# Performance work log

Hardware: AMD Instinct MI355X
Metric: run time of the kernel (lower is better)

## Reference

```python
import jax, jax.numpy as jnp
import numpy as np


def _time_encoding(t, hidden_dim):
    # Sinusoidal continuous-time encoding: t [B,T] -> [B,T,H]
    half = hidden_dim // 2
    freqs = jnp.exp(-jnp.arange(half, dtype=t.dtype) * (np.log(10000.0) / half))
    ang = t[..., None] * freqs  # [B,T,half]
    return jnp.concatenate([jnp.sin(ang), jnp.cos(ang)], axis=-1)


def _gru(x_tbh, w_ih, w_hh, b_ih, b_hh):
    # PyTorch-convention GRU over time-major input [T,B,H]
    B = x_tbh.shape[1]
    H = w_hh.shape[1]
    h0 = jnp.zeros((B, H), x_tbh.dtype)

    def step(h, x):
        gi = x @ w_ih.T + b_ih
        gh = h @ w_hh.T + b_hh
        i_r, i_z, i_n = jnp.split(gi, 3, axis=-1)
        h_r, h_z, h_n = jnp.split(gh, 3, axis=-1)
        r = jax.nn.sigmoid(i_r + h_r)
        z = jax.nn.sigmoid(i_z + h_z)
        n = jnp.tanh(i_n + r * h_n)
        h_new = (1.0 - z) * n + z * h
        return h_new, h_new

    _, ys = jax.lax.scan(step, h0, x_tbh)
    return ys  # [T,B,H]


def setup_inputs():
    key = jax.random.key(0)
    ks = jax.random.split(key, 8)
    B, T, D, H = 32, 256, 64, 128
    x = jax.random.normal(ks[0], (B, T, D), jnp.float32)
    missing_mask = (jax.random.uniform(ks[1], (B, T, D)) < 0.5).astype(jnp.float32)
    visit_time = jnp.cumsum(jax.random.uniform(ks[2], (B, T), jnp.float32) * 2.0, axis=1)
    time_delta = jnp.zeros((B, T), jnp.float32)
    lengths = jax.random.randint(ks[3], (B,), T // 2, T + 1).astype(jnp.int32)
    lengths = lengths.at[0].set(T)  # pad_packed returns max(lengths) steps; pin to T
    sensor_embed = jax.random.normal(ks[4], (D, H), jnp.float32) * 0.02
    k = 1.0 / np.sqrt(H)
    gru_w_ih = jax.random.uniform(ks[5], (3 * H, H), jnp.float32, -k, k)
    gru_w_hh = jax.random.uniform(ks[6], (3 * H, H), jnp.float32, -k, k)
    gru_b_ih = jax.random.uniform(ks[7], (3 * H,), jnp.float32, -k, k)
    gru_b_hh = jnp.zeros((3 * H,), jnp.float32)
    return dict(x=x, missing_mask=missing_mask, visit_time=visit_time,
                time_delta=time_delta, lengths=lengths, sensor_embed=sensor_embed,
                gru_w_ih=gru_w_ih, gru_w_hh=gru_w_hh, gru_b_ih=gru_b_ih, gru_b_hh=gru_b_hh)


def reference(x, missing_mask, visit_time, time_delta, lengths, sensor_embed,
              gru_w_ih, gru_w_hh, gru_b_ih, gru_b_hh):
    B, T, D = x.shape
    H = sensor_embed.shape[1]
    observed = 1.0 - missing_mask                                   # [B,T,D]
    # sensor tokens: per-(t,sensor) embedding scaled by value, zeroed if missing
    sensor_tokens = x[..., None] * sensor_embed[None, None] * observed[..., None]  # [B,T,D,H]
    presence = observed.mean(axis=1)                                # [B,D]
    sim = jax.nn.relu(sensor_embed @ sensor_embed.T)                # [D,D]
    adj = presence[:, :, None] * presence[:, None, :] * sim[None]   # [B,D,D]
    adj = adj + jnp.eye(D, dtype=x.dtype)[None]
    adj = adj / jnp.maximum(adj.sum(axis=-1, keepdims=True), 1e-6)
    graph_tokens = jnp.einsum('bij,btjh->btih', adj, sensor_tokens) # [B,T,D,H]
    visit_repr = graph_tokens.mean(axis=2) + _time_encoding(visit_time, H)  # [B,T,H]
    # dropout is identity in eval mode
    ys = _gru(jnp.swapaxes(visit_repr, 0, 1), gru_w_ih, gru_w_hh, gru_b_ih, gru_b_hh)
    out = jnp.swapaxes(ys, 0, 1)                                    # [B,T,H]
    # pad_packed_sequence semantics: zeros beyond each sequence length
    mask = (jnp.arange(T)[None, :] < lengths[:, None])[..., None]
    return out * mask
```

## Files before the change

### kernel.cpp

```cpp
#include <hip/hip_runtime.h>
#include <hip/hip_bf16.h>

#define B_ 32
#define T_ 256
#define D_ 64
#define H_ 128
#define G_ 384

typedef _Float16 half8 __attribute__((ext_vector_type(8)));
typedef _Float16 half4v __attribute__((ext_vector_type(4)));
typedef float float4v __attribute__((ext_vector_type(4)));

__device__ __forceinline__ float fsigmoid(float x){ return 1.0f/(1.0f+__expf(-x)); }
__device__ __forceinline__ float ftanh_(float x){ return 1.0f - 2.0f/(1.0f+__expf(2.0f*x)); }

#define BAR() do{ asm volatile("s_waitcnt lgkmcnt(0)" ::: "memory"); \
                  __builtin_amdgcn_s_barrier(); \
                  asm volatile("" ::: "memory"); } while(0)

__global__ void __launch_bounds__(256) adj_k(const float* mm, const float* E,
                                             float* wcol){
  int b = blockIdx.x;
  int tid = threadIdx.x;
  int d = tid & 63, q = tid >> 6;
  __shared__ float spp[4][64];
  __shared__ float sp[64];
  __shared__ float sE[64*129];
  __shared__ float ssim[64*65];
  __shared__ float srs[64];
  float p = 0.0f;
  for (int t = q*64; t < q*64+64; t++) p += 1.0f - mm[(b*T_ + t)*D_ + d];
  spp[q][d] = p;
  for (int i = tid; i < D_*H_; i += 256){ int r = i >> 7, c = i & 127; sE[r*129+c] = E[i]; }
  __syncthreads();
  if (tid < 64) sp[tid] = (spp[0][tid]+spp[1][tid]+spp[2][tid]+spp[3][tid]) * (1.0f/T_);
  __syncthreads();
  float rowE[128];
  #pragma unroll
  for (int k = 0; k < 128; k++) rowE[k] = sE[d*129+k];
  for (int i = q*16; i < q*16+16; i++){
    float s = 0.0f;
    #pragma unroll
    for (int k = 0; k < 128; k++) s += rowE[k]*sE[i*129+k];
    ssim[d*65+i] = fmaxf(s, 0.0f);
  }
  __syncthreads();
  if (tid < 64){
    float rs = 0.0f;
    for (int j = 0; j < 64; j++) rs += sp[j]*ssim[tid*65+j];
    srs[tid] = fmaxf(sp[tid]*rs + 1.0f, 1e-6f);
  }
  __syncthreads();
  if (tid < 64){
    float s = 0.0f;
    for (int i = 0; i < 64; i++) s += sp[i]*ssim[tid*65+i]/srs[i];
    wcol[b*64 + tid] = sp[tid]*s + 1.0f/srs[tid];
  }
}

#define AVP 72
#define VRP 136
#define SEP 132
__global__ void __launch_bounds__(512,1) gi_k(const float* x, const float* mm,
                                              const float* vt, const float* E,
                                              const float* wih, const float* bih,
                                              const float* bhh, const float* wcol,
                                              _Float16* gi3){
  int bid = blockIdx.x;
  int b = bid >> 3, t0 = (bid & 7)*32;
  int tid = threadIdx.x;
  int w = tid >> 6, l = tid & 63;
  int lq = l >> 4, lm = l & 15;

  __shared__ __align__(16) _Float16 av[32*AVP];
  __shared__ __align__(16) _Float16 vrA[32*VRP];
  __shared__ __align__(16) _Float16 sEl[64*SEP];
  __shared__ float sVt[32];

  {
    int i = tid*4, t = i >> 6, d4 = i & 63;
    long src = (long)(b*T_ + t0 + t)*D_ + d4;
    float4 xv = *(const float4*)&x[src];
    float4 mv = *(const float4*)&mm[src];
    float4 wv = *(const float4*)&wcol[b*D_ + d4];
    half4v h;
    h[0]=(_Float16)(xv.x*(1.0f-mv.x)*wv.x*(1.0f/64));
    h[1]=(_Float16)(xv.y*(1.0f-mv.y)*wv.y*(1.0f/64));
    h[2]=(_Float16)(xv.z*(1.0f-mv.z)*wv.z*(1.0f/64));
    h[3]=(_Float16)(xv.w*(1.0f-mv.w)*wv.w*(1.0f/64));
    *(half4v*)&av[t*AVP + d4] = h;
  }
  {
    int r = tid >> 3, c0 = (tid & 7)*16;
    #pragma unroll
    for (int g = 0; g < 4; g++){
      float4 v = *(const float4*)&E[r*H_ + c0 + g*4];
      half4v h;
      h[0]=(_Float16)v.x; h[1]=(_Float16)v.y; h[2]=(_Float16)v.z; h[3]=(_Float16)v.w;
      *(half4v*)&sEl[r*SEP + c0 + g*4] = h;
    }
  }
  if (tid < 32) sVt[tid] = vt[b*T_ + t0 + tid];
  __syncthreads();

  half8 bE[2];
  #pragma unroll
  for (int kc = 0; kc < 2; kc++){
    half8 f;
    #pragma unroll
    for (int jj = 0; jj < 8; jj++)
      f[jj] = sEl[(kc*32 + lq*8 + jj)*SEP + 16*w + lm];
    bE[kc] = f;
  }

  float4v accA[2] = {{0,0,0,0},{0,0,0,0}};
  #pragma unroll
  for (int kc = 0; kc < 2; kc++){
    #pragma unroll
    for (int mt = 0; mt < 2; mt++){
      half8 a = *(const half8*)&av[(mt*16+lm)*AVP + kc*32 + lq*8];
      accA[mt] = __builtin_amdgcn_mfma_f32_16x16x32_f16(a, bE[kc], accA[mt], 0,0,0);
    }
  }
  {
    int h = 16*w + lm;
    float fr = __expf(-(float)(h & 63) * 0.14391157f);
    #pragma unroll
    for (int mt = 0; mt < 2; mt++){
      #pragma unroll
      for (int r = 0; r < 4; r++){
        int tl = mt*16 + lq*4 + r;
        float ang = sVt[tl] * fr;
        float e = (h < 64) ? __sinf(ang) : __cosf(ang);
        vrA[tl*VRP + h] = (_Float16)(accA[mt][r] + e);
      }
    }
  }
  __syncthreads();

  half8 bW[3][4]; float biW[3];
  #pragma unroll
  for (int q = 0; q < 3; q++){
    int g = 16*(3*w + q) + lm;
    biW[q] = bih[g] + (g < 2*H_ ? bhh[g] : 0.0f);
    #pragma unroll
    for (int kc = 0; kc < 4; kc++){
      const float* src = &wih[(long)g*H_ + kc*32 + lq*8];
      float4 x0 = *(const float4*)src;
      float4 x1 = *(const float4*)(src+4);
      half8 f;
      f[0]=(_Float16)x0.x; f[1]=(_Float16)x0.y; f[2]=(_Float16)x0.z; f[3]=(_Float16)x0.w;
      f[4]=(_Float16)x1.x; f[5]=(_Float16)x1.y; f[6]=(_Float16)x1.z; f[7]=(_Float16)x1.w;
      bW[q][kc] = f;
    }
  }
  float4v cB[2][3];
  #pragma unroll
  for (int mt = 0; mt < 2; mt++)
    #pragma unroll
    for (int q = 0; q < 3; q++) cB[mt][q] = (float4v){0,0,0,0};
  #pragma unroll
  for (int kc = 0; kc < 4; kc++){
    #pragma unroll
    for (int mt = 0; mt < 2; mt++){
      half8 a = *(const half8*)&vrA[(mt*16+lm)*VRP + kc*32 + lq*8];
      #pragma unroll
      for (int q = 0; q < 3; q++)
        cB[mt][q] = __builtin_amdgcn_mfma_f32_16x16x32_f16(a, bW[q][kc], cB[mt][q], 0,0,0);
    }
  }
  #pragma unroll
  for (int mt = 0; mt < 2; mt++){
    #pragma unroll
    for (int q = 0; q < 3; q++){
      int g = 16*(3*w + q) + lm;
      int tb = t0 + mt*16 + lq*4;
      half4v hv;
      hv[0]=(_Float16)(cB[mt][q][0] + biW[q]); hv[1]=(_Float16)(cB[mt][q][1] + biW[q]);
      hv[2]=(_Float16)(cB[mt][q][2] + biW[q]); hv[3]=(_Float16)(cB[mt][q][3] + biW[q]);
      *(half4v*)&gi3[((long)(b*G_ + g))*T_ + tb] = hv;
    }
  }
}

__global__ void __launch_bounds__(256,1) gru_k(const _Float16* gi3, const float* whh,
                                               const float* bhh, const int* lengths,
                                               float* out){
  int b = blockIdx.x;
  int tid = threadIdx.x;
  int w = tid >> 6, l = tid & 63;
  int lq = l >> 4, lm = l & 15;
  int len = lengths[b];
  bool gate = (l < 32);
  int j = 32*w + l;

  __shared__ __align__(16) _Float16 hb[2][H_];

  half8 bfrag[6][4];
  #pragma unroll
  for (int i = 0; i < 6; i++){
    int row = 32*w + (i>>1)*H_ + (i&1)*16 + lm;
    #pragma unroll
    for (int kc = 0; kc < 4; kc++){
      const float* src = &whh[(long)row*H_ + kc*32 + lq*8];
      float4 x0 = *(const float4*)src;
      float4 x1 = *(const float4*)(src+4);
      half8 f;
      f[0]=(_Float16)x0.x; f[1]=(_Float16)x0.y; f[2]=(_Float16)x0.z; f[3]=(_Float16)x0.w;
      f[4]=(_Float16)x1.x; f[5]=(_Float16)x1.y; f[6]=(_Float16)x1.z; f[7]=(_Float16)x1.w;
      bfrag[i][kc] = f;
    }
  }
  float bn_ = 0.0f;
  const _Float16* pr = nullptr; const _Float16* pz; const _Float16* pn;
  if (gate){
    bn_ = bhh[2*H_ + j];
    pr = gi3 + ((long)b*G_ + j)*T_;
    pz = pr + (long)H_*T_;
    pn = pr + (long)2*H_*T_;
  }
  if (tid < H_){ hb[0][tid] = (_Float16)0.0f; hb[1][tid] = (_Float16)0.0f; }

  float gr[2][8], gz[2][8], gn[2][8];
  if (gate){
    half8 a = *(const half8*)(pr);
    half8 bv = *(const half8*)(pz);
    half8 cv = *(const half8*)(pn);
    #pragma unroll
    for (int i = 0; i < 8; i++){ gr[0][i]=(float)a[i]; gz[0][i]=(float)bv[i]; gn[0][i]=(float)cv[i]; }
  }
  __syncthreads();

  float hval = 0.0f;
  float ho[8];
  int cb = 0;
  for (int c = 0; c < 32; c++){
    if (gate && c+1 < 32){
      int nb2 = (c+1)*8;
      half8 a = *(const half8*)(pr+nb2);
      half8 bv = *(const half8*)(pz+nb2);
      half8 cv = *(const half8*)(pn+nb2);
      int nc = cb^1;
      #pragma unroll
      for (int i = 0; i < 8; i++){ gr[nc][i]=(float)a[i]; gz[nc][i]=(float)bv[i]; gn[nc][i]=(float)cv[i]; }
    }
    #pragma unroll
    for (int i = 0; i < 8; i++){
      int rp = i & 1;
      half8 a0v = *(const half8*)&hb[rp][0*32 + lq*8];
      half8 a1v = *(const half8*)&hb[rp][1*32 + lq*8];
      half8 a2v = *(const half8*)&hb[rp][2*32 + lq*8];
      half8 a3v = *(const half8*)&hb[rp][3*32 + lq*8];
      float4v cc[6];
      #pragma unroll
      for (int q = 0; q < 6; q++) cc[q] = (float4v){0,0,0,0};
      #pragma unroll
      for (int q = 0; q < 6; q++) cc[q] = __builtin_amdgcn_mfma_f32_16x16x32_f16(a0v, bfrag[q][0], cc[q], 0,0,0);
      #pragma unroll
      for (int q = 0; q < 6; q++) cc[q] = __builtin_amdgcn_mfma_f32_16x16x32_f16(a1v, bfrag[q][1], cc[q], 0,0,0);
      #pragma unroll
      for (int q = 0; q < 6; q++) cc[q] = __builtin_amdgcn_mfma_f32_16x16x32_f16(a2v, bfrag[q][2], cc[q], 0,0,0);
      #pragma unroll
      for (int q = 0; q < 6; q++) cc[q] = __builtin_amdgcn_mfma_f32_16x16x32_f16(a3v, bfrag[q][3], cc[q], 0,0,0);
      float ghr = (l & 16) ? cc[1][0] : cc[0][0];
      float ghz = (l & 16) ? cc[3][0] : cc[2][0];
      float ghn = (l & 16) ? cc[5][0] : cc[4][0];
      if (gate){
        float r = fsigmoid(gr[cb][i] + ghr);
        float z = fsigmoid(gz[cb][i] + ghz);
        float n = ftanh_(gn[cb][i] + r*(ghn + bn_));
        hval = (1.0f - z)*n + z*hval;
        hb[rp^1][j] = (_Float16)hval;
        ho[i] = (c*8 + i < len) ? hval : 0.0f;
      }
      BAR();
    }
    if (gate){
      long ob = ((long)b*T_ + c*8)*H_ + j;
      #pragma unroll
      for (int i = 0; i < 8; i++) out[ob + (long)i*H_] = ho[i];
    }
    cb ^= 1;
  }
}

extern "C" void kernel_launch(void* const* d_in, const int* in_sizes, int n_in,
                              void* d_out, int out_size, void* d_ws, size_t ws_size,
                              hipStream_t stream) {
  char* base = (char*)d_ws;
  size_t off = 0;
  auto alloc = [&](size_t bytes)->void*{
    void* p = base + off; off = (off + bytes + 255) & ~(size_t)255; return p;
  };
  float*     wcol = (float*)alloc((size_t)B_*D_*4);
  _Float16*  gi3  = (_Float16*)alloc((size_t)B_*G_*T_*2);
  if (off > ws_size) return;

  const float* x   = (const float*)d_in[0];
  const float* mm  = (const float*)d_in[1];
  const float* vt  = (const float*)d_in[2];
  const int*   len = (const int*)d_in[4];
  const float* E   = (const float*)d_in[5];
  const float* wih = (const float*)d_in[6];
  const float* whh = (const float*)d_in[7];
  const float* bih = (const float*)d_in[8];
  const float* bhh = (const float*)d_in[9];

  adj_k<<<dim3(B_),dim3(256),0,stream>>>(mm, E, wcol);
  gi_k<<<dim3(256),dim3(512),0,stream>>>(x, mm, vt, E, wih, bih, bhh, wcol, gi3);
  gru_k<<<dim3(B_),dim3(256),0,stream>>>(gi3, whh, bhh, len, (float*)d_out);
}
```

Baseline: 256.6 us.

## Split GRU recurrent matmul K dimension across two wave groups

Doubles the GRU block to 512 threads and splits the hidden-state reduction across two groups of four waves. Each group computes half of the recurrent matmul, writes partial sums to shared memory, and the first group combines them before the gate math. This aims to shorten the per-step MFMA dependency chain in the latency-bound recurrence. In exchange it adds an extra barrier and LDS round trip per timestep.

```diff
diff --git a/kernel.cpp b/kernel.cpp
--- a/kernel.cpp
+++ b/kernel.cpp
@@ -10,6 +10,7 @@
 typedef _Float16 half8 __attribute__((ext_vector_type(8)));
 typedef _Float16 half4v __attribute__((ext_vector_type(4)));
 typedef float float4v __attribute__((ext_vector_type(4)));
+typedef float float2v __attribute__((ext_vector_type(2)));
 
 __device__ __forceinline__ float fsigmoid(float x){ return 1.0f/(1.0f+__expf(-x)); }
 __device__ __forceinline__ float ftanh_(float x){ return 1.0f - 2.0f/(1.0f+__expf(2.0f*x)); }
@@ -183,32 +184,37 @@
   }
 }
 
-__global__ void __launch_bounds__(256,1) gru_k(const _Float16* gi3, const float* whh,
+__global__ void __launch_bounds__(512,1) gru_k(const _Float16* gi3, const float* whh,
                                                const float* bhh, const int* lengths,
                                                float* out){
   int b = blockIdx.x;
   int tid = threadIdx.x;
   int w = tid >> 6, l = tid & 63;
+  int ww = w & 3, kh = w >> 2;
   int lq = l >> 4, lm = l & 15;
   int len = lengths[b];
-  bool gate = (l < 32);
-  int j = 32*w + l;
+  bool part = (l < 32);
+  bool gate = part && (kh == 0);
+  int j = 32*ww + l;
 
   __shared__ __align__(16) _Float16 hb[2][H_];
-
-  half8 bfrag[6][4];
+  __shared__ __align__(16) float2v ghrz[2][H_];
+  __shared__ float ghn_[2][H_];
+
+  half8 bfrag[6][2];
   #pragma unroll
   for (int i = 0; i < 6; i++){
-    int row = 32*w + (i>>1)*H_ + (i&1)*16 + lm;
-    #pragma unroll
-    for (int kc = 0; kc < 4; kc++){
+    int row = 32*ww + (i>>1)*H_ + (i&1)*16 + lm;
+    #pragma unroll
+    for (int k2 = 0; k2 < 2; k2++){
+      int kc = 2*kh + k2;
       const float* src = &whh[(long)row*H_ + kc*32 + lq*8];
       float4 x0 = *(const float4*)src;
       float4 x1 = *(const float4*)(src+4);
       half8 f;
       f[0]=(_Float16)x0.x; f[1]=(_Float16)x0.y; f[2]=(_Float16)x0.z; f[3]=(_Float16)x0.w;
       f[4]=(_Float16)x1.x; f[5]=(_Float16)x1.y; f[6]=(_Float16)x1.z; f[7]=(_Float16)x1.w;
-      bfrag[i][kc] = f;
+      bfrag[i][k2] = f;
     }
   }
   float bn_ = 0.0f;
@@ -247,10 +253,8 @@
     #pragma unroll
     for (int i = 0; i < 8; i++){
       int rp = i & 1;
-      half8 a0v = *(const half8*)&hb[rp][0*32 + lq*8];
-      half8 a1v = *(const half8*)&hb[rp][1*32 + lq*8];
-      half8 a2v = *(const half8*)&hb[rp][2*32 + lq*8];
-      half8 a3v = *(const half8*)&hb[rp][3*32 + lq*8];
+      half8 a0v = *(const half8*)&hb[rp][kh*64 + 0*32 + lq*8];
+      half8 a1v = *(const half8*)&hb[rp][kh*64 + 1*32 + lq*8];
       float4v cc[6];
       #pragma unroll
       for (int q = 0; q < 6; q++) cc[q] = (float4v){0,0,0,0};
@@ -258,17 +262,20 @@
       for (int q = 0; q < 6; q++) cc[q] = __builtin_amdgcn_mfma_f32_16x16x32_f16(a0v, bfrag[q][0], cc[q], 0,0,0);
       #pragma unroll
       for (int q = 0; q < 6; q++) cc[q] = __builtin_amdgcn_mfma_f32_16x16x32_f16(a1v, bfrag[q][1], cc[q], 0,0,0);
-      #pragma unroll
-      for (int q = 0; q < 6; q++) cc[q] = __builtin_amdgcn_mfma_f32_16x16x32_f16(a2v, bfrag[q][2], cc[q], 0,0,0);
-      #pragma unroll
-      for (int q = 0; q < 6; q++) cc[q] = __builtin_amdgcn_mfma_f32_16x16x32_f16(a3v, bfrag[q][3], cc[q], 0,0,0);
-      float ghr = (l & 16) ? cc[1][0] : cc[0][0];
-      float ghz = (l & 16) ? cc[3][0] : cc[2][0];
-      float ghn = (l & 16) ? cc[5][0] : cc[4][0];
+      if (part){
+        float pr_ = (l & 16) ? cc[1][0] : cc[0][0];
+        float pz_ = (l & 16) ? cc[3][0] : cc[2][0];
+        float pn_ = (l & 16) ? cc[5][0] : cc[4][0];
+        ghrz[kh][j] = (float2v){pr_, pz_};
+        ghn_[kh][j] = pn_;
+      }
+      BAR();
       if (gate){
-        float r = fsigmoid(gr[cb][i] + ghr);
-        float z = fsigmoid(gz[cb][i] + ghz);
-        float n = ftanh_(gn[cb][i] + r*(ghn + bn_));
+        float2v rz0 = ghrz[0][j], rz1 = ghrz[1][j];
+        float n0 = ghn_[0][j],  n1 = ghn_[1][j];
+        float r = fsigmoid(gr[cb][i] + rz0[0] + rz1[0]);
+        float z = fsigmoid(gz[cb][i] + rz0[1] + rz1[1]);
+        float n = ftanh_(gn[cb][i] + r*(n0 + n1 + bn_));
         hval = (1.0f - z)*n + z*hval;
         hb[rp^1][j] = (_Float16)hval;
         ho[i] = (c*8 + i < len) ? hval : 0.0f;
@@ -308,5 +315,5 @@
 
   adj_k<<<dim3(B_),dim3(256),0,stream>>>(mm, E, wcol);
   gi_k<<<dim3(256),dim3(512),0,stream>>>(x, mm, vt, E, wih, bih, bhh, wcol, gi3);
-  gru_k<<<dim3(B_),dim3(256),0,stream>>>(gi3, whh, bhh, len, (float*)d_out);
+  gru_k<<<dim3(B_),dim3(512),0,stream>>>(gi3, whh, bhh, len, (float*)d_out);
 }
```

Result: slower. 268.1 us (+4.5%).
